# Kernel tuning notes

Measured on AMD Instinct MI355X. Metric: run time of the kernel, lower is better.

## Reference

```python
import jax, jax.numpy as jnp
import numpy as np

C = 256
CQK = C // 8


def setup_inputs() -> dict:
    key = jax.random.key(0)
    ks = jax.random.split(key, 8)
    B, H, W = 4, 64, 64
    x = jax.random.normal(ks[0], (B, C, H, W), dtype=jnp.float32)
    # 1x1 conv weights are plain [out_c, in_c] matrices + bias
    sq = 1.0 / np.sqrt(C)
    Wq = jax.random.uniform(ks[1], (CQK, C), jnp.float32, -sq, sq)
    bq = jax.random.uniform(ks[2], (CQK,), jnp.float32, -sq, sq)
    Wk = jax.random.uniform(ks[3], (CQK, C), jnp.float32, -sq, sq)
    bk = jax.random.uniform(ks[4], (CQK,), jnp.float32, -sq, sq)
    Wv = jax.random.uniform(ks[5], (C, C), jnp.float32, -sq, sq)
    bv = jax.random.uniform(ks[6], (C,), jnp.float32, -sq, sq)
    gamma = jnp.zeros((1,), dtype=jnp.float32)
    return {"x": x, "Wq": Wq, "bq": bq, "Wk": Wk, "bk": bk, "Wv": Wv, "bv": bv, "gamma": gamma}


def reference(x, Wq, bq, Wk, bk, Wv, bv, gamma):
    B, Cc, H, W = x.shape
    N = H * W
    xf = x.reshape(B, Cc, N)  # [B, C, N]
    # 1x1 convs == channel GEMMs
    q = jnp.einsum('dc,bcn->bdn', Wq, xf) + bq[None, :, None]  # [B, C/8, N]
    k = jnp.einsum('dc,bcn->bdn', Wk, xf) + bk[None, :, None]  # [B, C/8, N]
    v = jnp.einsum('dc,bcn->bdn', Wv, xf) + bv[None, :, None]  # [B, C, N]
    # attention[b, i, j] = softmax_j( q_i . k_j )  (no scaling, as in source)
    attn = jax.nn.softmax(jnp.einsum('bdn,bdm->bnm', q, k), axis=-1)  # [B, N, N]
    # out = value @ attention  (note: NOT attention^T, faithful to source)
    out = jnp.einsum('bcn,bnm->bcm', v, attn)  # [B, C, N]
    out = out.reshape(B, Cc, H, W)
    return gamma[0] * out + x
```

## Files before the change

### kernel.cpp

```cpp
#include <hip/hip_runtime.h>
#include <hip/hip_bf16.h>


#define NB 4
#define CC 256
#define NN 4096
#define L2E 1.44269504088896340f

typedef short  short4v  __attribute__((ext_vector_type(4)));
typedef short  short8v  __attribute__((ext_vector_type(8)));
typedef __bf16 bf16x8   __attribute__((ext_vector_type(8)));
typedef float  f32x4    __attribute__((ext_vector_type(4)));
typedef float  f32x16   __attribute__((ext_vector_type(16)));
typedef unsigned long u64x2 __attribute__((ext_vector_type(2)));
typedef unsigned int u32;

#define AS1 __attribute__((address_space(1)))
#define AS3 __attribute__((address_space(3)))

static __device__ __forceinline__ void gload16(const void* g, void* l) {
  __builtin_amdgcn_global_load_lds((const AS1 u32*)g, (AS3 u32*)l, 16, 0, 0);
}

static __device__ __forceinline__ unsigned short f2bf(float f) {
  union { __bf16 h; unsigned short u; } v; v.h = (__bf16)f; return v.u;
}

union FragU { short8v s; bf16x8 b; unsigned u[4]; };

static __device__ __forceinline__ bf16x8 ld_frag(const unsigned short* p) {
  FragU u; u.s = *(const short8v*)p; return u.b;
}

static __device__ __forceinline__ f32x16 zero16() {
  f32x16 v;
#pragma unroll
  for (int i = 0; i < 16; ++i) v[i] = 0.0f;
  return v;
}

static __device__ __forceinline__ f32x16 mfma32(bf16x8 a, bf16x8 b, f32x16 c) {
  return __builtin_amdgcn_mfma_f32_32x32x16_bf16(a, b, c, 0, 0, 0);
}

__global__ __launch_bounds__(256) void k_wcvt(
    const float* __restrict__ Wq, const float* __restrict__ Wk,
    const float* __restrict__ Wv, unsigned short* __restrict__ Wb)
{
  const int i4 = blockIdx.x * 256 + threadIdx.x;
  const int e = i4 * 4;
  const int row = e >> 8, c = e & 255;
  const float* src = (row < 32) ? (Wq + row * 256 + c)
                   : (row < 64) ? (Wk + (row - 32) * 256 + c)
                                : (Wv + (row - 64) * 256 + c);
  f32x4 v = *(const f32x4*)src;
  short4v s;
#pragma unroll
  for (int j = 0; j < 4; ++j) s[j] = (short)f2bf(v[j]);
  *(short4v*)(Wb + e) = s;
}

__global__ __launch_bounds__(256) void k_proj(
    const float* __restrict__ x, const unsigned short* __restrict__ Wb,
    const float* __restrict__ bq, const float* __restrict__ bk,
    const float* __restrict__ bv,
    unsigned short* __restrict__ Qt, unsigned short* __restrict__ Kt,
    unsigned char* __restrict__ V8)
{
  __shared__ unsigned short xs[32][268];
  const int t = threadIdx.x;
  const int b = blockIdx.y;
  const int n0 = blockIdx.x * 32;
  const int w = t >> 6, l = t & 63, h = l >> 5, col = l & 31;

  const float* xb = x + (size_t)b * CC * NN;
  {
    const int c_off = t >> 3, nl = 4 * (t & 7);
#pragma unroll
    for (int c0 = 0; c0 < CC; c0 += 32) {
      int c = c0 + c_off;
      f32x4 v4 = *(const f32x4*)(xb + (size_t)c * NN + n0 + nl);
#pragma unroll
      for (int j = 0; j < 4; ++j) xs[nl + j][c] = f2bf(v4[j]);
    }
  }
  __syncthreads();

  for (int f = w; f < 10; f += 4) {
    const float* bsrc; int rowbase; int mode; int wrow;
    if (f == 0)      { bsrc = bq; rowbase = 0;            mode = 0; wrow = 0; }
    else if (f == 1) { bsrc = bk; rowbase = 0;            mode = 1; wrow = 32; }
    else             { bsrc = bv; rowbase = (f - 2) * 32; mode = 2; wrow = 64 + rowbase; }

    f32x16 acc0 = zero16();
    const unsigned short* wr = Wb + (size_t)(wrow + col) * 256 + 8 * h;

#pragma unroll
    for (int k0 = 0; k0 < CC; k0 += 16) {
      FragU a;
      a.s = *(const short8v*)(wr + k0);
      const unsigned short* p0 = &xs[col][k0 + 8 * h];
      FragU b0;
      short4v t0a = *(const short4v*)p0, t0b = *(const short4v*)(p0 + 4);
#pragma unroll
      for (int j = 0; j < 4; ++j) { b0.s[j] = t0a[j]; b0.s[4 + j] = t0b[j]; }
      acc0 = mfma32(a.b, b0.b, acc0);
    }

    const int n = n0 + col;
#pragma unroll
    for (int q = 0; q < 4; ++q) {
      f32x4 bias4 = *(const f32x4*)(bsrc + rowbase + 8 * q + 4 * h);
      float vals[4];
#pragma unroll
      for (int i = 0; i < 4; ++i) vals[i] = acc0[4 * q + i] + bias4[i];
      if (mode == 2) {
        const size_t tb = (((size_t)b * (NN >> 4) + (n >> 4)) * 2 + ((n >> 3) & 1)) * CC * 8
                          + (n & 7);
        u32 w01 = __builtin_amdgcn_cvt_pk_fp8_f32(vals[0], vals[1], 0, false);
        u32 w23 = __builtin_amdgcn_cvt_pk_fp8_f32(vals[2], vals[3], 0, false);
        const int cb0 = rowbase + 8 * q + 4 * h;
        V8[tb + (size_t)(cb0 + 0) * 8] = (unsigned char)(w01 & 0xff);
        V8[tb + (size_t)(cb0 + 1) * 8] = (unsigned char)((w01 >> 8) & 0xff);
        V8[tb + (size_t)(cb0 + 2) * 8] = (unsigned char)(w23 & 0xff);
        V8[tb + (size_t)(cb0 + 3) * 8] = (unsigned char)((w23 >> 8) & 0xff);
      } else {
        unsigned short* dst = (mode == 0) ? Qt : Kt;
        const float scale = (mode == 0) ? L2E : 1.0f;
        short4v s4;
#pragma unroll
        for (int i = 0; i < 4; ++i) s4[i] = (short)f2bf(vals[i] * scale);
        *(short4v*)(dst + ((size_t)b * NN + n) * 32 + 8 * q + 4 * h) = s4;
      }
    }
  }
}

__global__ __launch_bounds__(256) void k_rowstats(
    const unsigned short* __restrict__ Qt, const unsigned short* __restrict__ Kt,
    float* __restrict__ cbias)
{
  __shared__ float ssum[4][32];
  const int t = threadIdx.x;
  const int w = t >> 6, l = t & 63, h = l >> 5, col = l & 31;
  const int b = blockIdx.y;
  const int n0 = blockIdx.x * 32;
  const unsigned short* Qb = Qt + (size_t)b * NN * 32;
  const unsigned short* Kb = Kt + (size_t)b * NN * 32;

  bf16x8 bq0 = ld_frag(Qb + (size_t)(n0 + col) * 32 + 8 * h);
  bf16x8 bq1 = ld_frag(Qb + (size_t)(n0 + col) * 32 + 16 + 8 * h);

  float acc = 0.0f;
  const int mbase = w * (NN / 4);
#pragma unroll 2
  for (int mt = 0; mt < 32; ++mt) {
    const int m0 = mbase + mt * 32;
    bf16x8 ak0 = ld_frag(Kb + (size_t)(m0 + col) * 32 + 8 * h);
    bf16x8 ak1 = ld_frag(Kb + (size_t)(m0 + col) * 32 + 16 + 8 * h);
    f32x16 S = zero16();
    S = mfma32(ak0, bq0, S);
    S = mfma32(ak1, bq1, S);
    float p0 = 0.0f, p1 = 0.0f, p2 = 0.0f, p3 = 0.0f;
#pragma unroll
    for (int r = 0; r < 4; ++r) {
      p0 += __builtin_amdgcn_exp2f(S[r]);
      p1 += __builtin_amdgcn_exp2f(S[4 + r]);
      p2 += __builtin_amdgcn_exp2f(S[8 + r]);
      p3 += __builtin_amdgcn_exp2f(S[12 + r]);
    }
    acc += (p0 + p1) + (p2 + p3);
  }
  acc += __shfl_xor(acc, 32);

  if (l < 32) ssum[w][l] = acc;
  __syncthreads();

  if (t < 32) {
    float s = (ssum[0][t] + ssum[1][t]) + (ssum[2][t] + ssum[3][t]);
    cbias[(size_t)b * NN + n0 + t] = -__builtin_amdgcn_logf(s);
  }
}

__global__ __launch_bounds__(512) void k_attn_out(
    const unsigned short* __restrict__ Qt, const unsigned short* __restrict__ Kt,
    const unsigned char* __restrict__ V8,
    const float* __restrict__ cbias,
    float* __restrict__ pout,
    int nsplit, int nlen)
{
  __shared__ __align__(16) char qbuf[2][2][2048];
  __shared__ __align__(16) char vbuf[3][2][8192];
  __shared__ __align__(16) char ebuf[2][2][4096];

  const int wg = (int)blockIdx.x;
  const int chunk = (int)gridDim.x >> 3;
  const int id2 = (wg & 7) * chunk + (wg >> 3);
  const int per_b = 32 * nsplit;
  const int b = id2 / per_b;
  const int rem = id2 - b * per_b;
  const int ns = rem >> 5;
  const int m0 = (rem & 31) * 128;
  const int nbeg = ns * nlen;

  const int t = threadIdx.x;
  const int w = t >> 6, l = t & 63, h = l >> 5, col = l & 31;
  const int mfp = w & 3;
  const int ccons = (w & 3) * 64;

  const unsigned short* Kb = Kt + (size_t)b * NN * 32;
  const float* cb = cbias + (size_t)b * NN + nbeg;

  bf16x8 bk0 = ld_frag(Kb + (size_t)(m0 + 32 * mfp + col) * 32 + 8 * h);
  bf16x8 bk1 = ld_frag(Kb + (size_t)(m0 + 32 * mfp + col) * 32 + 16 + 8 * h);

  const int ll = l & 15;
  const size_t gqoff = (size_t)(((w & 1) * 16 + ll) * 64 + ((w >> 1) & 1) * 16
                                + (w >> 2) * 32);
  const char* qsrc = (const char*)Qt + ((size_t)b * NN + nbeg) * 64 + gqoff;
  const char* vsrc = (const char*)V8 + ((size_t)b * (NN >> 4) + (nbeg >> 4)) * 4096
                     + (size_t)t * 16;

  f32x16 acc[4][2];
#pragma unroll
  for (int mf = 0; mf < 4; ++mf)
#pragma unroll
    for (int cf = 0; cf < 2; ++cf) acc[mf][cf] = zero16();

  const int J = nlen >> 6;

  if (ll == l) {
    gload16(qsrc, &qbuf[0][0][w * 256]);
    gload16(qsrc + 2048, &qbuf[0][1][w * 256]);
  }
  gload16(vsrc, &vbuf[0][0][w * 1024]);
  gload16(vsrc + 8192, &vbuf[0][1][w * 1024]);
  __syncthreads();

  for (int j = 0; j <= J; ++j) {
    if (j + 1 < J) {
      const size_t qoff = (size_t)(2 * j + 2) * 2048;
      const size_t voff = (size_t)(2 * j + 2) * 8192;
      const int qs = (j + 1) & 1, vs = (j + 1) % 3;
      if (ll == l) {
        gload16(qsrc + qoff, &qbuf[qs][0][w * 256]);
        gload16(qsrc + qoff + 2048, &qbuf[qs][1][w * 256]);
      }
      gload16(vsrc + voff, &vbuf[vs][0][w * 1024]);
      gload16(vsrc + voff + 8192, &vbuf[vs][1][w * 1024]);
    }

    if (w < 4) {
      if (j < J) {
#pragma unroll
        for (int u = 0; u < 2; ++u) {
          const char* qb = &qbuf[j & 1][u][0];
          FragU fq0, fq1;
          fq0.s = *(const short8v*)(qb + l * 16);
          fq1.s = *(const short8v*)(qb + 1024 + l * 16);
          f32x16 S = zero16();
          S = mfma32(fq0.b, bk0, S);
          S = mfma32(fq1.b, bk1, S);

          float e[16];
          const float* cbi = cb + (2 * j + u) * 32;
#pragma unroll
          for (int q = 0; q < 4; ++q) {
            f32x4 cb4 = *(const f32x4*)(cbi + 8 * q + 4 * h);
#pragma unroll
            for (int i = 0; i < 4; ++i)
              e[4 * q + i] = __builtin_amdgcn_exp2f(S[4 * q + i] + cb4[i]);
          }
          u32 wA = __builtin_amdgcn_cvt_pk_fp8_f32(e[0], e[1], 0, false);
          wA = __builtin_amdgcn_cvt_pk_fp8_f32(e[2], e[3], wA, true);
          u32 wB = __builtin_amdgcn_cvt_pk_fp8_f32(e[4], e[5], 0, false);
          wB = __builtin_amdgcn_cvt_pk_fp8_f32(e[6], e[7], wB, true);
          u32 wC = __builtin_amdgcn_cvt_pk_fp8_f32(e[8], e[9], 0, false);
          wC = __builtin_amdgcn_cvt_pk_fp8_f32(e[10], e[11], wC, true);
          u32 wD = __builtin_amdgcn_cvt_pk_fp8_f32(e[12], e[13], 0, false);
          wD = __builtin_amdgcn_cvt_pk_fp8_f32(e[14], e[15], wD, true);
          asm("v_permlane32_swap_b32 %0, %1" : "+v"(wA), "+v"(wB));
          asm("v_permlane32_swap_b32 %0, %1" : "+v"(wC), "+v"(wD));
          u64x2 ev;
          ev[0] = ((unsigned long)wB << 32) | wA;
          ev[1] = ((unsigned long)wD << 32) | wC;
          *(u64x2*)(&ebuf[j & 1][u][mfp * 1024 + l * 16]) = ev;
        }
      }
    } else {
      if (j > 0) {
        const int pv = (j + 2) % 3;
        __builtin_amdgcn_s_setprio(1);
#pragma unroll
        for (int u = 0; u < 2; ++u) {
          const char* vb = &vbuf[pv][u][h * 2048 + (ccons + col) * 8];
          long v00 = *(const long*)(vb);
          long v01 = *(const long*)(vb + 256);
          long v10 = *(const long*)(vb + 4096);
          long v11 = *(const long*)(vb + 4096 + 256);
          const char* eb = &ebuf[(j - 1) & 1][u][l * 16];
#pragma unroll
          for (int mf = 0; mf < 4; ++mf) {
            u64x2 ev = *(const u64x2*)(eb + mf * 1024);
            acc[mf][0] = __builtin_amdgcn_mfma_f32_32x32x16_fp8_fp8(
                (long)ev[0], v00, acc[mf][0], 0, 0, 0);
            acc[mf][0] = __builtin_amdgcn_mfma_f32_32x32x16_fp8_fp8(
                (long)ev[1], v10, acc[mf][0], 0, 0, 0);
            acc[mf][1] = __builtin_amdgcn_mfma_f32_32x32x16_fp8_fp8(
                (long)ev[0], v01, acc[mf][1], 0, 0, 0);
            acc[mf][1] = __builtin_amdgcn_mfma_f32_32x32x16_fp8_fp8(
                (long)ev[1], v11, acc[mf][1], 0, 0, 0);
          }
        }
        __builtin_amdgcn_s_setprio(0);
      }
    }

    if (j < J) __syncthreads();
  }

  if (w >= 4) {
    float* pb = pout + (((size_t)ns * NB + b) * NN + m0) * CC + ccons;
#pragma unroll
    for (int mf = 0; mf < 4; ++mf)
#pragma unroll
      for (int cf = 0; cf < 2; ++cf)
#pragma unroll
        for (int r = 0; r < 16; ++r) {
          int mloc = 32 * mf + (r & 3) + 8 * (r >> 2) + 4 * h;
          pb[(size_t)mloc * CC + 32 * cf + col] = acc[mf][cf][r];
        }
  }
}

__global__ __launch_bounds__(256) void k_comb(
    const float* __restrict__ pout, const float* __restrict__ x,
    const float* __restrict__ gamma, float* __restrict__ out, int nsplit)
{
  __shared__ float ld[64][65];
  const size_t STRIDE = (size_t)NB * CC * NN;
  const int t = threadIdx.x;
  const int m0 = blockIdx.x * 64, c0 = blockIdx.y * 64, b = blockIdx.z;
  const int ci = t & 63, mo = t >> 6;

  const float* pb = pout + ((size_t)b * NN + m0) * CC + c0;
#pragma unroll
  for (int rep = 0; rep < 16; ++rep) {
    const int mi = 4 * rep + mo;
    float s = pb[(size_t)mi * CC + ci];
    for (int ns = 1; ns < nsplit; ++ns)
      s += pb[ns * STRIDE + (size_t)mi * CC + ci];
    ld[mi][ci] = s;
  }
  __syncthreads();

  const float g = gamma[0];
  const int mi2 = t & 63;
#pragma unroll
  for (int rep = 0; rep < 16; ++rep) {
    const int cj = 4 * rep + mo;
    const size_t idx = ((size_t)b * CC + c0 + cj) * NN + m0 + mi2;
    out[idx] = g * ld[mi2][cj] + x[idx];
  }
}

extern "C" void kernel_launch(void* const* d_in, const int* in_sizes, int n_in,
                              void* d_out, int out_size, void* d_ws, size_t ws_size,
                              hipStream_t stream) {
  const float* x     = (const float*)d_in[0];
  const float* Wq    = (const float*)d_in[1];
  const float* bq    = (const float*)d_in[2];
  const float* Wk    = (const float*)d_in[3];
  const float* bk    = (const float*)d_in[4];
  const float* Wv    = (const float*)d_in[5];
  const float* bv    = (const float*)d_in[6];
  const float* gamma = (const float*)d_in[7];
  float* out = (float*)d_out;

  char* ws = (char*)d_ws;
  unsigned short* Qt = (unsigned short*)(ws);
  unsigned short* Kt = (unsigned short*)(ws + (1u << 20));
  unsigned char*  V8 = (unsigned char*)(ws + (2u << 20));
  unsigned short* Wb = (unsigned short*)(ws + (6u << 20));
  float* cbias = (float*)(ws + (10u << 20) + (2u << 18));
  const size_t POUT_OFF = (11u << 20);
  float* pout = (float*)(ws + POUT_OFF);
  const size_t PART_BYTES = (size_t)NB * CC * NN * 4;

  int nsplit = (ws_size >= POUT_OFF + 2 * PART_BYTES) ? 2 : 1;

  k_wcvt<<<dim3(80), 256, 0, stream>>>(Wq, Wk, Wv, Wb);
  k_proj<<<dim3(NN / 32, NB), 256, 0, stream>>>(x, Wb, bq, bk, bv, Qt, Kt, V8);
  k_rowstats<<<dim3(NN / 32, NB), 256, 0, stream>>>(Qt, Kt, cbias);
  k_attn_out<<<dim3(128 * nsplit), 512, 0, stream>>>(
      Qt, Kt, V8, cbias, pout, nsplit, NN / nsplit);
  k_comb<<<dim3(NN / 64, CC / 64, NB), 256, 0, stream>>>(pout, x, gamma, out, nsplit);
}
```

Measured before the change: 95.87 us.

## Double per-iteration attention chunk, store bf16 partials, reorder fp8 MFMA chain

Each pipeline step of the attention-output kernel now handles 128 keys instead of 64, halving the number of barriers and loop iterations at the cost of about twice the LDS footprint (roughly 160KB per block). The fp8 MFMA sequence is interleaved across the four m-fragments so independent accumulators hide MFMA dependency latency. Partial outputs are written and read as bf16 instead of fp32, halving the traffic of the partial buffer between the attention and combine kernels at some precision cost. The larger LDS use may limit occupancy.

```diff
diff --git a/kernel.cpp b/kernel.cpp
--- a/kernel.cpp
+++ b/kernel.cpp
@@ -24,6 +24,9 @@
 
 static __device__ __forceinline__ unsigned short f2bf(float f) {
   union { __bf16 h; unsigned short u; } v; v.h = (__bf16)f; return v.u;
+}
+static __device__ __forceinline__ float bf2f(unsigned short u) {
+  union { unsigned u; float f; } v; v.u = (u32)u << 16; return v.f;
 }
 
 union FragU { short8v s; bf16x8 b; unsigned u[4]; };
@@ -186,12 +189,12 @@
     const unsigned short* __restrict__ Qt, const unsigned short* __restrict__ Kt,
     const unsigned char* __restrict__ V8,
     const float* __restrict__ cbias,
-    float* __restrict__ pout,
+    unsigned short* __restrict__ pout,
     int nsplit, int nlen)
 {
-  __shared__ __align__(16) char qbuf[2][2][2048];
-  __shared__ __align__(16) char vbuf[3][2][8192];
-  __shared__ __align__(16) char ebuf[2][2][4096];
+  __shared__ __align__(16) char qbuf[2][4][2048];
+  __shared__ __align__(16) char vbuf[3][4][8192];
+  __shared__ __align__(16) char ebuf[2][4][4096];
 
   const int wg = (int)blockIdx.x;
   const int chunk = (int)gridDim.x >> 3;
@@ -227,33 +230,31 @@
 #pragma unroll
     for (int cf = 0; cf < 2; ++cf) acc[mf][cf] = zero16();
 
-  const int J = nlen >> 6;
-
-  if (ll == l) {
-    gload16(qsrc, &qbuf[0][0][w * 256]);
-    gload16(qsrc + 2048, &qbuf[0][1][w * 256]);
-  }
-  gload16(vsrc, &vbuf[0][0][w * 1024]);
-  gload16(vsrc + 8192, &vbuf[0][1][w * 1024]);
+  const int J = nlen >> 7;
+
+#pragma unroll
+  for (int u = 0; u < 4; ++u) {
+    if (ll == l) gload16(qsrc + (size_t)u * 2048, &qbuf[0][u][w * 256]);
+    gload16(vsrc + (size_t)u * 8192, &vbuf[0][u][w * 1024]);
+  }
   __syncthreads();
 
   for (int j = 0; j <= J; ++j) {
     if (j + 1 < J) {
-      const size_t qoff = (size_t)(2 * j + 2) * 2048;
-      const size_t voff = (size_t)(2 * j + 2) * 8192;
+      const size_t qoff = (size_t)(4 * j + 4) * 2048;
+      const size_t voff = (size_t)(4 * j + 4) * 8192;
       const int qs = (j + 1) & 1, vs = (j + 1) % 3;
-      if (ll == l) {
-        gload16(qsrc + qoff, &qbuf[qs][0][w * 256]);
-        gload16(qsrc + qoff + 2048, &qbuf[qs][1][w * 256]);
+#pragma unroll
+      for (int u = 0; u < 4; ++u) {
+        if (ll == l) gload16(qsrc + qoff + (size_t)u * 2048, &qbuf[qs][u][w * 256]);
+        gload16(vsrc + voff + (size_t)u * 8192, &vbuf[vs][u][w * 1024]);
       }
-      gload16(vsrc + voff, &vbuf[vs][0][w * 1024]);
-      gload16(vsrc + voff + 8192, &vbuf[vs][1][w * 1024]);
     }
 
     if (w < 4) {
       if (j < J) {
 #pragma unroll
-        for (int u = 0; u < 2; ++u) {
+        for (int u = 0; u < 4; ++u) {
           const char* qb = &qbuf[j & 1][u][0];
           FragU fq0, fq1;
           fq0.s = *(const short8v*)(qb + l * 16);
@@ -263,7 +264,7 @@
           S = mfma32(fq1.b, bk1, S);
 
           float e[16];
-          const float* cbi = cb + (2 * j + u) * 32;
+          const float* cbi = cb + (4 * j + u) * 32;
 #pragma unroll
           for (int q = 0; q < 4; ++q) {
             f32x4 cb4 = *(const f32x4*)(cbi + 8 * q + 4 * h);
@@ -292,25 +293,33 @@
         const int pv = (j + 2) % 3;
         __builtin_amdgcn_s_setprio(1);
 #pragma unroll
-        for (int u = 0; u < 2; ++u) {
+        for (int u = 0; u < 4; ++u) {
           const char* vb = &vbuf[pv][u][h * 2048 + (ccons + col) * 8];
           long v00 = *(const long*)(vb);
           long v01 = *(const long*)(vb + 256);
           long v10 = *(const long*)(vb + 4096);
           long v11 = *(const long*)(vb + 4096 + 256);
           const char* eb = &ebuf[(j - 1) & 1][u][l * 16];
-#pragma unroll
-          for (int mf = 0; mf < 4; ++mf) {
-            u64x2 ev = *(const u64x2*)(eb + mf * 1024);
-            acc[mf][0] = __builtin_amdgcn_mfma_f32_32x32x16_fp8_fp8(
-                (long)ev[0], v00, acc[mf][0], 0, 0, 0);
-            acc[mf][0] = __builtin_amdgcn_mfma_f32_32x32x16_fp8_fp8(
-                (long)ev[1], v10, acc[mf][0], 0, 0, 0);
-            acc[mf][1] = __builtin_amdgcn_mfma_f32_32x32x16_fp8_fp8(
-                (long)ev[0], v01, acc[mf][1], 0, 0, 0);
-            acc[mf][1] = __builtin_amdgcn_mfma_f32_32x32x16_fp8_fp8(
-                (long)ev[1], v11, acc[mf][1], 0, 0, 0);
-          }
+          u64x2 ev0 = *(const u64x2*)(eb);
+          u64x2 ev1 = *(const u64x2*)(eb + 1024);
+          u64x2 ev2 = *(const u64x2*)(eb + 2048);
+          u64x2 ev3 = *(const u64x2*)(eb + 3072);
+          acc[0][0] = __builtin_amdgcn_mfma_f32_32x32x16_fp8_fp8((long)ev0[0], v00, acc[0][0], 0, 0, 0);
+          acc[1][0] = __builtin_amdgcn_mfma_f32_32x32x16_fp8_fp8((long)ev1[0], v00, acc[1][0], 0, 0, 0);
+          acc[2][0] = __builtin_amdgcn_mfma_f32_32x32x16_fp8_fp8((long)ev2[0], v00, acc[2][0], 0, 0, 0);
+          acc[3][0] = __builtin_amdgcn_mfma_f32_32x32x16_fp8_fp8((long)ev3[0], v00, acc[3][0], 0, 0, 0);
+          acc[0][1] = __builtin_amdgcn_mfma_f32_32x32x16_fp8_fp8((long)ev0[0], v01, acc[0][1], 0, 0, 0);
+          acc[1][1] = __builtin_amdgcn_mfma_f32_32x32x16_fp8_fp8((long)ev1[0], v01, acc[1][1], 0, 0, 0);
+          acc[2][1] = __builtin_amdgcn_mfma_f32_32x32x16_fp8_fp8((long)ev2[0], v01, acc[2][1], 0, 0, 0);
+          acc[3][1] = __builtin_amdgcn_mfma_f32_32x32x16_fp8_fp8((long)ev3[0], v01, acc[3][1], 0, 0, 0);
+          acc[0][0] = __builtin_amdgcn_mfma_f32_32x32x16_fp8_fp8((long)ev0[1], v10, acc[0][0], 0, 0, 0);
+          acc[1][0] = __builtin_amdgcn_mfma_f32_32x32x16_fp8_fp8((long)ev1[1], v10, acc[1][0], 0, 0, 0);
+          acc[2][0] = __builtin_amdgcn_mfma_f32_32x32x16_fp8_fp8((long)ev2[1], v10, acc[2][0], 0, 0, 0);
+          acc[3][0] = __builtin_amdgcn_mfma_f32_32x32x16_fp8_fp8((long)ev3[1], v10, acc[3][0], 0, 0, 0);
+          acc[0][1] = __builtin_amdgcn_mfma_f32_32x32x16_fp8_fp8((long)ev0[1], v11, acc[0][1], 0, 0, 0);
+          acc[1][1] = __builtin_amdgcn_mfma_f32_32x32x16_fp8_fp8((long)ev1[1], v11, acc[1][1], 0, 0, 0);
+          acc[2][1] = __builtin_amdgcn_mfma_f32_32x32x16_fp8_fp8((long)ev2[1], v11, acc[2][1], 0, 0, 0);
+          acc[3][1] = __builtin_amdgcn_mfma_f32_32x32x16_fp8_fp8((long)ev3[1], v11, acc[3][1], 0, 0, 0);
         }
         __builtin_amdgcn_s_setprio(0);
       }
@@ -320,7 +329,7 @@
   }
 
   if (w >= 4) {
-    float* pb = pout + (((size_t)ns * NB + b) * NN + m0) * CC + ccons;
+    unsigned short* pb = pout + (((size_t)ns * NB + b) * NN + m0) * CC + ccons;
 #pragma unroll
     for (int mf = 0; mf < 4; ++mf)
 #pragma unroll
@@ -328,13 +337,13 @@
 #pragma unroll
         for (int r = 0; r < 16; ++r) {
           int mloc = 32 * mf + (r & 3) + 8 * (r >> 2) + 4 * h;
-          pb[(size_t)mloc * CC + 32 * cf + col] = acc[mf][cf][r];
+          pb[(size_t)mloc * CC + 32 * cf + col] = f2bf(acc[mf][cf][r]);
         }
   }
 }
 
 __global__ __launch_bounds__(256) void k_comb(
-    const float* __restrict__ pout, const float* __restrict__ x,
+    const unsigned short* __restrict__ pout, const float* __restrict__ x,
     const float* __restrict__ gamma, float* __restrict__ out, int nsplit)
 {
   __shared__ float ld[64][65];
@@ -343,13 +352,13 @@
   const int m0 = blockIdx.x * 64, c0 = blockIdx.y * 64, b = blockIdx.z;
   const int ci = t & 63, mo = t >> 6;
 
-  const float* pb = pout + ((size_t)b * NN + m0) * CC + c0;
+  const unsigned short* pb = pout + ((size_t)b * NN + m0) * CC + c0;
 #pragma unroll
   for (int rep = 0; rep < 16; ++rep) {
     const int mi = 4 * rep + mo;
-    float s = pb[(size_t)mi * CC + ci];
+    float s = bf2f(pb[(size_t)mi * CC + ci]);
     for (int ns = 1; ns < nsplit; ++ns)
-      s += pb[ns * STRIDE + (size_t)mi * CC + ci];
+      s += bf2f(pb[ns * STRIDE + (size_t)mi * CC + ci]);
     ld[mi][ci] = s;
   }
   __syncthreads();
@@ -384,8 +393,8 @@
   unsigned short* Wb = (unsigned short*)(ws + (6u << 20));
   float* cbias = (float*)(ws + (10u << 20) + (2u << 18));
   const size_t POUT_OFF = (11u << 20);
-  float* pout = (float*)(ws + POUT_OFF);
-  const size_t PART_BYTES = (size_t)NB * CC * NN * 4;
+  unsigned short* pout = (unsigned short*)(ws + POUT_OFF);
+  const size_t PART_BYTES = (size_t)NB * CC * NN * 2;
 
   int nsplit = (ws_size >= POUT_OFF + 2 * PART_BYTES) ? 2 : 1;
 
```

Result: slower. 98.16 us (+2.4%).
